# Performance work log

Measured on AMD Instinct MI355X. Metric: run time of the kernel, lower is better.

The kernel has to match this reference:

```python
import jax, jax.numpy as jnp
import numpy as np

THRESHOLD = 8.0
B, C, H, W = 16, 512, 56, 56


def setup_inputs() -> dict:
    key = jax.random.key(0)
    # scale by 3 so per-channel max|x| ~ 13 > threshold -> channels disassemble with T=2
    x = jax.random.normal(key, (B, C, H, W), dtype=jnp.float32) * 3.0
    return {"x": x}


def _plan(x):
    """Host-side plan (mirrors the .item() host sync in the torch module).
    Returns outlier channel ids, the gather index that replicates each outlier
    channel T times, and the matching 1/T scale per output channel."""
    xv = np.asarray(x)
    max_vals = np.max(np.abs(xv), axis=(0, 2, 3))              # [C] per-channel max|x|
    outlier_idx = np.nonzero(max_vals > THRESHOLD)[0]          # channels to disassemble
    T = np.ceil(max_vals[outlier_idx] / THRESHOLD).astype(np.int64)
    rep_idx = np.repeat(outlier_idx, T)                        # each outlier channel repeated T times
    inv_T = np.repeat((1.0 / T).astype(np.float32), T)         # per-output-channel scale 1/T
    return outlier_idx, rep_idx, inv_T


def reference(x):
    outlier_idx, rep_idx, inv_T = _plan(x)
    rep = jnp.asarray(rep_idx)
    scale = jnp.asarray(inv_T)
    # single fused gather + scale replaces the per-channel slice/divide/repeat/concat loop
    disassembled_x = x[:, rep, :, :] * scale[None, :, None, None]
    return disassembled_x, jnp.asarray(outlier_idx)
```

## Files before the change

kernel.cpp:

```cpp
#include <hip/hip_runtime.h>

#define CH    512
#define BATCH 16
#define QB    4
#define NQ    (BATCH / QB)
#define HW    3136
#define HW4   784
#define THRESH 8.0f

typedef float f4 __attribute__((ext_vector_type(4)));

__global__ __launch_bounds__(256) void absmax_kernel(const float* __restrict__ x,
                                                     float* __restrict__ partial) {
    const int c   = blockIdx.x;
    const int q   = blockIdx.y;
    const int tid = threadIdx.x;
    float m = 0.0f;
    for (int bb = 0; bb < QB; ++bb) {
        const int b = q * QB + bb;
        const f4* src = reinterpret_cast<const f4*>(x) + (size_t)(b * CH + c) * HW4;
        for (int p = tid; p < HW4; p += 256) {
            f4 v = src[p];
            m = fmaxf(m, fmaxf(fmaxf(fabsf(v.x), fabsf(v.y)),
                               fmaxf(fabsf(v.z), fabsf(v.w))));
        }
    }
    __shared__ float sm[256];
    sm[tid] = m;
    __syncthreads();
    for (int off = 128; off > 0; off >>= 1) {
        if (tid < off) sm[tid] = fmaxf(sm[tid], sm[tid + off]);
        __syncthreads();
    }
    if (tid == 0) partial[c * NQ + q] = sm[0];
}

__global__ __launch_bounds__(256) void gather_kernel(const float* __restrict__ x,
                                                     const float* __restrict__ partial,
                                                     float* __restrict__ out,
                                                     float* __restrict__ out_tail,
                                                     int R) {
    const int nwg  = gridDim.x;
    const int orig = blockIdx.x;
    const int xcd  = orig & 7;
    const int q8 = nwg >> 3, r8 = nwg & 7;
    const int wg = (xcd < r8 ? xcd * (q8 + 1) : r8 * (q8 + 1) + (xcd - r8) * q8)
                   + (orig >> 3);
    const int j = wg >> 4;
    const int b = wg & 15;

    const int tid  = threadIdx.x;
    const int lane = tid & 63;
    const int w    = tid >> 6;

    const int c0 = tid * 2, c1 = c0 + 1;
    f4 p0 = reinterpret_cast<const f4*>(partial)[tid * 2];
    f4 p1 = reinterpret_cast<const f4*>(partial)[tid * 2 + 1];
    float m0 = fmaxf(fmaxf(p0.x, p0.y), fmaxf(p0.z, p0.w));
    float m1 = fmaxf(fmaxf(p1.x, p1.y), fmaxf(p1.z, p1.w));
    int T0 = (m0 > THRESH) ? (int)ceilf(m0 * 0.125f) : 0;
    int T1 = (m1 > THRESH) ? (int)ceilf(m1 * 0.125f) : 0;
    const int v = T0 + T1;

    int s = v;
    #pragma unroll
    for (int off = 1; off < 64; off <<= 1) {
        int t2 = __shfl_up(s, off, 64);
        if (lane >= off) s += t2;
    }
    __shared__ int wsum[4];
    if (lane == 63) wsum[w] = s;
    __syncthreads();
    int woff = 0;
    #pragma unroll
    for (int k = 0; k < 4; ++k) if (k < w) woff += wsum[k];
    const int excl   = woff + s - v;
    const int start0 = excl, start1 = excl + T0;

    __shared__ int sc, sT;
    if (T0 > 0 && j >= start0 && j < start0 + T0) { sc = c0; sT = T0; }
    if (T1 > 0 && j >= start1 && j < start1 + T1) { sc = c1; sT = T1; }

    if (wg == 0) {
        const int o0 = (T0 > 0), o1 = (T1 > 0);
        const int v2 = o0 + o1;
        int s2 = v2;
        #pragma unroll
        for (int off = 1; off < 64; off <<= 1) {
            int t2 = __shfl_up(s2, off, 64);
            if (lane >= off) s2 += t2;
        }
        __shared__ int wsum2[4];
        if (lane == 63) wsum2[w] = s2;
        __syncthreads();
        int woff2 = 0;
        #pragma unroll
        for (int k = 0; k < 4; ++k) if (k < w) woff2 += wsum2[k];
        const int ex2 = woff2 + s2 - v2;
        if (o0) out_tail[ex2]      = (float)c0;
        if (o1) out_tail[ex2 + o0] = (float)c1;
    }
    __syncthreads();

    const int   c     = sc;
    const float scale = (float)(1.0 / (double)sT);

    const f4* src = reinterpret_cast<const f4*>(x) + (size_t)(b * CH + c) * HW4;
    f4* dst = reinterpret_cast<f4*>(out) + ((size_t)b * R + j) * HW4;
    for (int p = tid; p < HW4; p += 256) {
        f4 vv = src[p];
        vv.x *= scale; vv.y *= scale; vv.z *= scale; vv.w *= scale;
        __builtin_nontemporal_store(vv, &dst[p]);
    }
}

extern "C" void kernel_launch(void* const* d_in, const int* in_sizes, int n_in,
                              void* d_out, int out_size, void* d_ws, size_t ws_size,
                              hipStream_t stream) {
    const float* x = (const float*)d_in[0];
    float* out = (float*)d_out;

    const int plane = BATCH * HW;
    const int R     = out_size / plane;

    float* partial = (float*)d_ws;

    absmax_kernel<<<dim3(CH, NQ), 256, 0, stream>>>(x, partial);
    if (R > 0) {
        gather_kernel<<<dim3(R * BATCH), 256, 0, stream>>>(
            x, partial, out, out + (size_t)R * plane, R);
    }
}
```

Measured before the change: 66.62 us.

## Fuse absmax and gather into one cooperative persistent kernel with grid sync

Merges the per-channel absmax reduction and the replicated-channel gather into a single cooperative kernel of 1024 persistent blocks separated by a grid-wide sync. Each block builds a shared-memory table mapping output channel to source channel and T, then loops over output planes in a grid-stride pattern. The aim is to remove the second launch and let the gather reuse x while it may still be in cache from the reduction. The cost is a grid barrier, a fixed grid that must fit co-resident, and the loss of the XCD-aware block remapping.

After: 131.8 us. 1.98x slower.

```diff
diff --git a/kernel.cpp b/kernel.cpp
--- a/kernel.cpp
+++ b/kernel.cpp
@@ -1,63 +1,63 @@
 #include <hip/hip_runtime.h>
+#include <hip/hip_cooperative_groups.h>
+
+namespace cg = cooperative_groups;
 
 #define CH    512
 #define BATCH 16
-#define QB    4
-#define NQ    (BATCH / QB)
+#define NB    1024
+#define QB    8
+#define NQ    2
 #define HW    3136
 #define HW4   784
 #define THRESH 8.0f
+#define MAXR  3072
 
 typedef float f4 __attribute__((ext_vector_type(4)));
 
-__global__ __launch_bounds__(256) void absmax_kernel(const float* __restrict__ x,
-                                                     float* __restrict__ partial) {
-    const int c   = blockIdx.x;
-    const int q   = blockIdx.y;
+__global__ __launch_bounds__(256, 4) void fused_kernel(
+        const float* __restrict__ x,
+        float*       __restrict__ partial,
+        float*       __restrict__ out,
+        float*       __restrict__ out_tail,
+        int R) {
+    const int g   = blockIdx.x;
     const int tid = threadIdx.x;
-    float m = 0.0f;
-    for (int bb = 0; bb < QB; ++bb) {
-        const int b = q * QB + bb;
-        const f4* src = reinterpret_cast<const f4*>(x) + (size_t)(b * CH + c) * HW4;
-        for (int p = tid; p < HW4; p += 256) {
-            f4 v = src[p];
-            m = fmaxf(m, fmaxf(fmaxf(fabsf(v.x), fabsf(v.y)),
-                               fmaxf(fabsf(v.z), fabsf(v.w))));
-        }
-    }
-    __shared__ float sm[256];
-    sm[tid] = m;
-    __syncthreads();
-    for (int off = 128; off > 0; off >>= 1) {
-        if (tid < off) sm[tid] = fmaxf(sm[tid], sm[tid + off]);
-        __syncthreads();
-    }
-    if (tid == 0) partial[c * NQ + q] = sm[0];
-}
-
-__global__ __launch_bounds__(256) void gather_kernel(const float* __restrict__ x,
-                                                     const float* __restrict__ partial,
-                                                     float* __restrict__ out,
-                                                     float* __restrict__ out_tail,
-                                                     int R) {
-    const int nwg  = gridDim.x;
-    const int orig = blockIdx.x;
-    const int xcd  = orig & 7;
-    const int q8 = nwg >> 3, r8 = nwg & 7;
-    const int wg = (xcd < r8 ? xcd * (q8 + 1) : r8 * (q8 + 1) + (xcd - r8) * q8)
-                   + (orig >> 3);
-    const int j = wg >> 4;
-    const int b = wg & 15;
-
-    const int tid  = threadIdx.x;
     const int lane = tid & 63;
     const int w    = tid >> 6;
 
+    {
+        const int c = g >> 1, q = g & 1;
+        float m = 0.0f;
+        for (int bb = 0; bb < QB; ++bb) {
+            const int b = q * QB + bb;
+            const f4* src = reinterpret_cast<const f4*>(x) + (size_t)(b * CH + c) * HW4;
+            for (int p = tid; p < HW4; p += 256) {
+                f4 v = src[p];
+                m = fmaxf(m, fmaxf(fmaxf(fabsf(v.x), fabsf(v.y)),
+                                   fmaxf(fabsf(v.z), fabsf(v.w))));
+            }
+        }
+        __shared__ float sm[256];
+        sm[tid] = m;
+        __syncthreads();
+        for (int off = 128; off > 0; off >>= 1) {
+            if (tid < off) sm[tid] = fmaxf(sm[tid], sm[tid + off]);
+            __syncthreads();
+        }
+        if (tid == 0) partial[(c << 1) + q] = sm[0];
+    }
+
+    cg::this_grid().sync();
+
+    __shared__ unsigned short rep_c[MAXR];
+    __shared__ unsigned char  rep_T[MAXR];
+    __shared__ int wsum[4];
+
     const int c0 = tid * 2, c1 = c0 + 1;
-    f4 p0 = reinterpret_cast<const f4*>(partial)[tid * 2];
-    f4 p1 = reinterpret_cast<const f4*>(partial)[tid * 2 + 1];
-    float m0 = fmaxf(fmaxf(p0.x, p0.y), fmaxf(p0.z, p0.w));
-    float m1 = fmaxf(fmaxf(p1.x, p1.y), fmaxf(p1.z, p1.w));
+    f4 pp = reinterpret_cast<const f4*>(partial)[tid];
+    float m0 = fmaxf(pp.x, pp.y);
+    float m1 = fmaxf(pp.z, pp.w);
     int T0 = (m0 > THRESH) ? (int)ceilf(m0 * 0.125f) : 0;
     int T1 = (m1 > THRESH) ? (int)ceilf(m1 * 0.125f) : 0;
     const int v = T0 + T1;
@@ -68,20 +68,18 @@
         int t2 = __shfl_up(s, off, 64);
         if (lane >= off) s += t2;
     }
-    __shared__ int wsum[4];
     if (lane == 63) wsum[w] = s;
     __syncthreads();
     int woff = 0;
     #pragma unroll
     for (int k = 0; k < 4; ++k) if (k < w) woff += wsum[k];
-    const int excl   = woff + s - v;
-    const int start0 = excl, start1 = excl + T0;
+    const int start0 = woff + s - v;
+    const int start1 = start0 + T0;
+    for (int k = 0; k < T0; ++k) { rep_c[start0 + k] = (unsigned short)c0; rep_T[start0 + k] = (unsigned char)T0; }
+    for (int k = 0; k < T1; ++k) { rep_c[start1 + k] = (unsigned short)c1; rep_T[start1 + k] = (unsigned char)T1; }
 
-    __shared__ int sc, sT;
-    if (T0 > 0 && j >= start0 && j < start0 + T0) { sc = c0; sT = T0; }
-    if (T1 > 0 && j >= start1 && j < start1 + T1) { sc = c1; sT = T1; }
-
-    if (wg == 0) {
+    if (g == 0) {
+        __shared__ int wsum2[4];
         const int o0 = (T0 > 0), o1 = (T1 > 0);
         const int v2 = o0 + o1;
         int s2 = v2;
@@ -90,7 +88,6 @@
             int t2 = __shfl_up(s2, off, 64);
             if (lane >= off) s2 += t2;
         }
-        __shared__ int wsum2[4];
         if (lane == 63) wsum2[w] = s2;
         __syncthreads();
         int woff2 = 0;
@@ -102,15 +99,20 @@
     }
     __syncthreads();
 
-    const int   c     = sc;
-    const float scale = (float)(1.0 / (double)sT);
-
-    const f4* src = reinterpret_cast<const f4*>(x) + (size_t)(b * CH + c) * HW4;
-    f4* dst = reinterpret_cast<f4*>(out) + ((size_t)b * R + j) * HW4;
-    for (int p = tid; p < HW4; p += 256) {
-        f4 vv = src[p];
-        vv.x *= scale; vv.y *= scale; vv.z *= scale; vv.w *= scale;
-        __builtin_nontemporal_store(vv, &dst[p]);
+    const int total = R * BATCH;
+    for (int u = g; u < total; u += NB) {
+        const int j = u >> 4;
+        const int b = u & 15;
+        const int   c  = rep_c[j];
+        const int   T  = rep_T[j];
+        const float sc = (float)(1.0 / (double)T);
+        const f4* src = reinterpret_cast<const f4*>(x)   + (size_t)(b * CH + c) * HW4;
+        f4*       dst = reinterpret_cast<f4*>(out)       + ((size_t)b * R + j) * HW4;
+        for (int p = tid; p < HW4; p += 256) {
+            f4 vv = src[p];
+            vv.x *= sc; vv.y *= sc; vv.z *= sc; vv.w *= sc;
+            __builtin_nontemporal_store(vv, &dst[p]);
+        }
     }
 }
 
@@ -121,13 +123,12 @@
     float* out = (float*)d_out;
 
     const int plane = BATCH * HW;
-    const int R     = out_size / plane;
+    int R = out_size / plane;
 
-    float* partial = (float*)d_ws;
+    float* partial  = (float*)d_ws;
+    float* out_tail = out + (size_t)R * plane;
 
-    absmax_kernel<<<dim3(CH, NQ), 256, 0, stream>>>(x, partial);
-    if (R > 0) {
-        gather_kernel<<<dim3(R * BATCH), 256, 0, stream>>>(
-            x, partial, out, out + (size_t)R * plane, R);
-    }
+    void* args[] = { (void*)&x, (void*)&partial, (void*)&out, (void*)&out_tail, (void*)&R };
+    hipLaunchCooperativeKernel(reinterpret_cast<void*>(fused_kernel),
+                               dim3(NB), dim3(256), args, 0, stream);
 }
```
